# Kernel optimization log

Hardware: AMD Instinct MI355X
Metric: run time of the kernel (lower is better)

The kernel has to match this reference:

```python
import jax, jax.numpy as jnp
import numpy as np

B, D, T = 256, 128, 512
E, H, WH, WIN = 128, 512, 512, 64

def setup_inputs() -> dict:
    key = jax.random.key(0)
    ks = jax.random.split(key, 13)
    def rn(k, shape, scale=0.05):
        return jax.random.normal(k, shape, dtype=jnp.float32) * scale
    return {
        "z_ctx": rn(ks[0], (B, D, WIN), 1.0),
        "z": rn(ks[1], (B, D, T), 1.0),
        "z_slow": rn(ks[2], (B, D, T), 1.0),
        "z_fast": rn(ks[3], (B, D, T), 1.0),
        "e": rn(ks[4], (B, E), 1.0),
        "W_enc": rn(ks[5], (WH, D * WIN)),
        "b_enc": rn(ks[6], (WH,)),
        "W_ih": rn(ks[7], (3 * H, WH + E)),
        "W_hh": rn(ks[8], (3 * H, H)),
        "b_ih": rn(ks[9], (3 * H,)),
        "b_hh": rn(ks[10], (3 * H,)),
        "W_fc": rn(ks[11], (D, H)),
        "b_fc": rn(ks[12], (D,)),
    }

def reference(z_ctx, z, z_slow, z_fast, e, W_enc, b_enc, W_ih, W_hh, b_ih, b_hh, W_fc, b_fc):
    # teacher_forcing=False path (deterministic reference)
    Bb, Dd, Tt = z.shape
    # SlowWindowEncoder: flatten window + Linear + ReLU -> [B, WH]
    context = jax.nn.relu(z_ctx.reshape(Bb, -1) @ W_enc.T + b_enc)
    slow_input = jnp.concatenate([context, e], axis=-1)  # constant over t
    gi = slow_input @ W_ih.T + b_ih                      # [B, 3H], precomputed
    i_r, i_z, i_n = jnp.split(gi, 3, axis=-1)
    Hh = W_hh.shape[1]
    h0 = jnp.zeros((Bb, Hh), dtype=z.dtype)
    zp0 = z_ctx[:, :, -1]                                # z_slow_prev init

    def step(carry, _):
        h, zp = carry
        gh = h @ W_hh.T + b_hh
        h_r, h_z, h_n = jnp.split(gh, 3, axis=-1)
        r = jax.nn.sigmoid(i_r + h_r)
        zg = jax.nn.sigmoid(i_z + h_z)
        n = jnp.tanh(i_n + r * h_n)
        h_new = (1.0 - zg) * n + zg * h                  # GRUCell update
        zh = zp + h_new @ W_fc.T + b_fc                  # residual delta
        return (h_new, zh), zh

    _, zs = jax.lax.scan(step, (h0, zp0), None, length=Tt)  # [T, B, D]
    return jnp.transpose(zs, (1, 2, 0))                  # [B, D, T]
```

## Files before the change

### kernel.cpp

```cpp
#include <hip/hip_runtime.h>

typedef __attribute__((ext_vector_type(8))) short s8v;
typedef __attribute__((ext_vector_type(4))) float f4v;

#define MFMA16(a, b, c) __builtin_amdgcn_mfma_f32_16x16x32_bf16((a), (b), (c), 0, 0, 0)

__device__ __forceinline__ unsigned short f2bf(float f) {
  unsigned u = __float_as_uint(f);
  return (unsigned short)((u + 0x7fffu + ((u >> 16) & 1u)) >> 16);
}

__global__ void cvt4_kernel(const float* __restrict__ in, unsigned short* __restrict__ out, int n4) {
  int i = blockIdx.x * blockDim.x + threadIdx.x;
  if (i >= n4) return;
  float4 v = ((const float4*)in)[i];
  ushort4 o;
  o.x = f2bf(v.x); o.y = f2bf(v.y); o.z = f2bf(v.z); o.w = f2bf(v.w);
  ((ushort4*)out)[i] = o;
}

__global__ void build_slow_kernel(const float* __restrict__ context, const float* __restrict__ e,
                                  unsigned short* __restrict__ out) {
  int i = blockIdx.x * blockDim.x + threadIdx.x;
  if (i >= 256 * 640) return;
  int b = i / 640, c = i - b * 640;
  float v = (c < 512) ? context[b * 512 + c] : e[b * 128 + (c - 512)];
  out[i] = f2bf(v);
}

template <int RELU>
__global__ __launch_bounds__(256) void gemm_bt(const unsigned short* __restrict__ A,
                                               const unsigned short* __restrict__ B,
                                               const float* __restrict__ bias, float* __restrict__ C,
                                               int M, int N, int K) {
  __shared__ unsigned short As[64][48];
  __shared__ unsigned short Bs[64][48];
  int tid = threadIdx.x;
  int lane = tid & 63, w = tid >> 6;
  int m = lane & 15, q = lane >> 4;
  int row0 = blockIdx.x * 64, col0 = blockIdx.y * 64;
  int sr = tid >> 2, sk = (tid & 3) * 8;
  const unsigned short* Ap = A + (size_t)(row0 + sr) * K + sk;
  const unsigned short* Bp = B + (size_t)(col0 + sr) * K + sk;
  f4v acc[4];
#pragma unroll
  for (int nt = 0; nt < 4; nt++) acc[nt] = (f4v){0.f, 0.f, 0.f, 0.f};

  for (int k0 = 0; k0 < K; k0 += 32) {
    *(uint4*)&As[sr][sk] = *(const uint4*)(Ap + k0);
    *(uint4*)&Bs[sr][sk] = *(const uint4*)(Bp + k0);
    __syncthreads();
    s8v a = *(const s8v*)&As[w * 16 + m][q * 8];
#pragma unroll
    for (int nt = 0; nt < 4; nt++) {
      s8v bb = *(const s8v*)&Bs[nt * 16 + m][q * 8];
      acc[nt] = MFMA16(a, bb, acc[nt]);
    }
    __syncthreads();
  }
#pragma unroll
  for (int nt = 0; nt < 4; nt++) {
    int c = col0 + nt * 16 + m;
    float bv = bias[c];
#pragma unroll
    for (int i = 0; i < 4; i++) {
      int r = row0 + w * 16 + q * 4 + i;
      float v = acc[nt][i] + bv;
      if (RELU) v = v > 0.f ? v : 0.f;
      C[(size_t)r * N + c] = v;
    }
  }
}

__global__ __launch_bounds__(64) void gru_scan5(const float* __restrict__ gi,
                                                const unsigned short* __restrict__ Whh,
                                                const float* __restrict__ bhh,
                                                unsigned long long* __restrict__ Hall8,
                                                unsigned int* __restrict__ flags) {
  __shared__ unsigned short wlds[6 * 16 * 64 * 8];
  int tid = threadIdx.x;
  int bid = blockIdx.x;
  int bg = bid >> 4, cg = bid & 15;
  int b0 = bg * 16;
  int n = tid & 15, q = tid >> 4;

#pragma unroll 1
  for (int it = 0; it < 96; ++it) {
    int g = it >> 5, rem = it & 31, ct = rem >> 4, kc = rem & 15;
    int row = g * 512 + cg * 32 + ct * 16 + n;
    int kcol = kc * 32 + q * 8;
    *(uint4*)&wlds[(((g * 2 + ct) * 16 + kc) * 64 + tid) * 8] =
        *(const uint4*)(Whh + (size_t)row * 512 + kcol);
  }

  float gir[2][4], giz[2][4], gin[2][4], bhn[2][4];
#pragma unroll
  for (int ct = 0; ct < 2; ++ct) {
#pragma unroll
    for (int i = 0; i < 4; ++i) {
      int c = cg * 32 + ct * 16 + q * 4 + i;
      const float* gp = gi + (size_t)(b0 + n) * 1536 + c;
      gir[ct][i] = gp[0] + bhh[c];
      giz[ct][i] = gp[512] + bhh[c + 512];
      gin[ct][i] = gp[1024];
      bhn[ct][i] = bhh[c + 1024];
    }
  }
  float hp[2][4] = {{0.f, 0.f, 0.f, 0.f}, {0.f, 0.f, 0.f, 0.f}};
  __syncthreads();

  unsigned int* myflag = flags + bg * 32 + cg;
  const unsigned int* pollp = flags + bg * 32 + (tid & 15);
  size_t rowbase = (size_t)(b0 + n) * 512 * 128;

#pragma unroll 1
  for (int t = 0; t < 512; ++t) {
    f4v ar[2], az[2], an[2];
#pragma unroll
    for (int ct = 0; ct < 2; ++ct) {
      ar[ct] = (f4v){gir[ct][0], gir[ct][1], gir[ct][2], gir[ct][3]};
      az[ct] = (f4v){giz[ct][0], giz[ct][1], giz[ct][2], giz[ct][3]};
      an[ct] = (f4v){bhn[ct][0], bhn[ct][1], bhn[ct][2], bhn[ct][3]};
    }
    if (t > 0) {
      unsigned tgt = (unsigned)t;
      for (long sp = 0; sp < 500000L; ++sp) {
        unsigned v = __hip_atomic_load(pollp, __ATOMIC_RELAXED, __HIP_MEMORY_SCOPE_AGENT);
        if (__ballot(v >= tgt) == 0xffffffffffffffffULL) break;
        if ((sp & 8191) == 8191) __builtin_amdgcn_fence(__ATOMIC_ACQUIRE, "agent");
      }
      asm volatile("" ::: "memory");
      unsigned long long* hp8 = Hall8 + rowbase + (size_t)(t - 1) * 128 + q * 2;
      s8v bf[16];
#pragma unroll
      for (int kc = 0; kc < 16; ++kc) {
        union { unsigned long long u[2]; s8v v; } uv;
        uv.u[0] = __hip_atomic_load(hp8 + kc * 8, __ATOMIC_RELAXED, __HIP_MEMORY_SCOPE_AGENT);
        uv.u[1] = __hip_atomic_load(hp8 + kc * 8 + 1, __ATOMIC_RELAXED, __HIP_MEMORY_SCOPE_AGENT);
        bf[kc] = uv.v;
      }
#pragma unroll
      for (int kc = 0; kc < 16; ++kc) {
#pragma unroll
        for (int ct = 0; ct < 2; ++ct) {
          s8v a0 = *(const s8v*)&wlds[(((0 + ct) * 16 + kc) * 64 + tid) * 8];
          ar[ct] = MFMA16(a0, bf[kc], ar[ct]);
          s8v a1 = *(const s8v*)&wlds[(((2 + ct) * 16 + kc) * 64 + tid) * 8];
          az[ct] = MFMA16(a1, bf[kc], az[ct]);
          s8v a2 = *(const s8v*)&wlds[(((4 + ct) * 16 + kc) * 64 + tid) * 8];
          an[ct] = MFMA16(a2, bf[kc], an[ct]);
        }
      }
    }
#pragma unroll
    for (int ct = 0; ct < 2; ++ct) {
      union { unsigned short s[4]; unsigned long long u; } pk;
#pragma unroll
      for (int i = 0; i < 4; ++i) {
        float r = 1.f / (1.f + __expf(-ar[ct][i]));
        float zg = 1.f / (1.f + __expf(-az[ct][i]));
        float x = gin[ct][i] + r * an[ct][i];
        float ex = __expf(2.f * x);
        float nn = 1.f - 2.f / (ex + 1.f);
        float h = (1.f - zg) * nn + zg * hp[ct][i];
        hp[ct][i] = h;
        pk.s[i] = f2bf(h);
      }
      __hip_atomic_store(Hall8 + rowbase + (size_t)t * 128 + (size_t)(cg * 8 + ct * 4 + q), pk.u,
                         __ATOMIC_RELAXED, __HIP_MEMORY_SCOPE_AGENT);
    }
    asm volatile("s_waitcnt vmcnt(0)" ::: "memory");
    if (tid == 0)
      __hip_atomic_store(myflag, (unsigned int)(t + 1), __ATOMIC_RELAXED,
                         __HIP_MEMORY_SCOPE_AGENT);
  }
}

__global__ __launch_bounds__(256) void fc_scan(const unsigned short* __restrict__ Hall,
                                               const unsigned short* __restrict__ Wfc,
                                               const float* __restrict__ bfc,
                                               const float* __restrict__ zctx,
                                               float* __restrict__ out) {
  __shared__ unsigned short hs[16][520];
  int tid = threadIdx.x;
  int lane = tid & 63, w = tid >> 6;
  int m = lane & 15, q = lane >> 4;
  int b = blockIdx.x;

  s8v wf[2][16];
  float bf_r[2], carry[2];
#pragma unroll
  for (int j = 0; j < 2; j++) {
    int d = (2 * w + j) * 16 + m;
#pragma unroll
    for (int kc = 0; kc < 16; kc++)
      wf[j][kc] = *(const s8v*)(Wfc + (size_t)d * 512 + kc * 32 + q * 8);
    bf_r[j] = bfc[d];
    carry[j] = zctx[((size_t)b * 128 + d) * 64 + 63];
  }

#pragma unroll 1
  for (int chunk = 0; chunk < 32; chunk++) {
    int t0 = chunk * 16;
    {
      int mm = tid >> 4, ci = (tid & 15) * 4;
      const unsigned short* src = Hall + ((size_t)b * 512 + t0 + mm) * 512 + ci * 8;
#pragma unroll
      for (int o = 0; o < 4; o++) {
        uint4 v = *(const uint4*)(src + o * 8);
        *(uint4*)&hs[mm][(ci + o) * 8] = v;
      }
    }
    __syncthreads();
    s8v af[16];
#pragma unroll
    for (int kc = 0; kc < 16; kc++) af[kc] = *(const s8v*)&hs[m][kc * 32 + q * 8];
    f4v acc[2];
    acc[0] = (f4v){0.f, 0.f, 0.f, 0.f};
    acc[1] = (f4v){0.f, 0.f, 0.f, 0.f};
#pragma unroll
    for (int kc = 0; kc < 16; kc++) {
      acc[0] = MFMA16(af[kc], wf[0][kc], acc[0]);
      acc[1] = MFMA16(af[kc], wf[1][kc], acc[1]);
    }
    __syncthreads();

#pragma unroll
    for (int j = 0; j < 2; j++) {
      float s0 = acc[j][0] + bf_r[j];
      float s1 = s0 + acc[j][1] + bf_r[j];
      float s2 = s1 + acc[j][2] + bf_r[j];
      float s3 = s2 + acc[j][3] + bf_r[j];
      float tot = s3;
      float incl = tot;
      float u = __shfl_up(incl, 16, 64);
      if (q >= 1) incl += u;
      u = __shfl_up(incl, 32, 64);
      if (q >= 2) incl += u;
      float excl = incl - tot;
      float add = excl + carry[j];
      int d = (2 * w + j) * 16 + m;
      float4 o4 = make_float4(s0 + add, s1 + add, s2 + add, s3 + add);
      *(float4*)(out + ((size_t)b * 128 + d) * 512 + t0 + q * 4) = o4;
      float chunktot = __shfl(incl, 48 + m, 64);
      carry[j] += chunktot;
    }
  }
}

extern "C" void kernel_launch(void* const* d_in, const int* in_sizes, int n_in,
                              void* d_out, int out_size, void* d_ws, size_t ws_size,
                              hipStream_t stream) {
  const float* z_ctx = (const float*)d_in[0];
  const float* e     = (const float*)d_in[4];
  const float* W_enc = (const float*)d_in[5];
  const float* b_enc = (const float*)d_in[6];
  const float* W_ih  = (const float*)d_in[7];
  const float* W_hh  = (const float*)d_in[8];
  const float* b_ih  = (const float*)d_in[9];
  const float* b_hh  = (const float*)d_in[10];
  const float* W_fc  = (const float*)d_in[11];
  const float* b_fc  = (const float*)d_in[12];
  float* out = (float*)d_out;

  char* ws = (char*)d_ws;
  const size_t OFF_WENC = 0;
  const size_t OFF_ZCTX = 8388608;
  const size_t OFF_WIH  = 12582912;
  const size_t OFF_WHH  = 14548992;
  const size_t OFF_WFC  = 16121856;
  const size_t OFF_CTX  = 16252928;
  const size_t OFF_SLOW = 16777216;
  const size_t OFF_GI   = 17104896;
  const size_t OFF_HALL = 18677760;
  const size_t OFF_SYNC = OFF_HALL + 134217728ull;
  const size_t NEED = OFF_SYNC + 32768;
  if (ws_size < NEED) return;

  unsigned short* Wenc_bf = (unsigned short*)(ws + OFF_WENC);
  unsigned short* zctx_bf = (unsigned short*)(ws + OFF_ZCTX);
  unsigned short* Wih_bf  = (unsigned short*)(ws + OFF_WIH);
  unsigned short* Whh_bf  = (unsigned short*)(ws + OFF_WHH);
  unsigned short* Wfc_bf  = (unsigned short*)(ws + OFF_WFC);
  float* context          = (float*)(ws + OFF_CTX);
  unsigned short* slow_bf = (unsigned short*)(ws + OFF_SLOW);
  float* gi               = (float*)(ws + OFF_GI);
  unsigned short* Hall    = (unsigned short*)(ws + OFF_HALL);
  unsigned long long* Hall8 = (unsigned long long*)(ws + OFF_HALL);
  unsigned int* flags     = (unsigned int*)(ws + OFF_SYNC);

  hipMemsetAsync(flags, 0, 4096, stream);

  cvt4_kernel<<<4096, 256, 0, stream>>>(W_enc, Wenc_bf, 512 * 8192 / 4);
  cvt4_kernel<<<2048, 256, 0, stream>>>(z_ctx, zctx_bf, 256 * 8192 / 4);
  cvt4_kernel<<<960, 256, 0, stream>>>(W_ih, Wih_bf, 1536 * 640 / 4);
  cvt4_kernel<<<768, 256, 0, stream>>>(W_hh, Whh_bf, 1536 * 512 / 4);
  cvt4_kernel<<<64, 256, 0, stream>>>(W_fc, Wfc_bf, 128 * 512 / 4);

  gemm_bt<1><<<dim3(4, 8), 256, 0, stream>>>(zctx_bf, Wenc_bf, b_enc, context, 256, 512, 8192);
  build_slow_kernel<<<640, 256, 0, stream>>>(context, e, slow_bf);
  gemm_bt<0><<<dim3(4, 24), 256, 0, stream>>>(slow_bf, Wih_bf, b_ih, gi, 256, 1536, 640);

  {
    const float* gi_c = gi;
    const unsigned short* whh_c = Whh_bf;
    const float* bhh_c = b_hh;
    unsigned long long* hall_c = Hall8;
    unsigned int* flags_c = flags;
    void* args[] = {(void*)&gi_c, (void*)&whh_c, (void*)&bhh_c, (void*)&hall_c, (void*)&flags_c};
    hipError_t err = hipLaunchCooperativeKernel((void*)gru_scan5, dim3(256), dim3(64), args, 0, stream);
    if (err != hipSuccess) {
      gru_scan5<<<256, 64, 0, stream>>>(gi, Whh_bf, b_hh, Hall8, flags);
    }
  }

  fc_scan<<<256, 256, 0, stream>>>(Hall, Wfc_bf, b_fc, z_ctx, out);
}
```

Before: 2.497 ms.

## Widen GRU scan hidden-state exchange and flag polling to 16-byte cache-bypassing accesses

The recurrent GRU kernel now exchanges hidden state between blocks with 16-byte global loads and stores carrying sc0 sc1 bits, replacing pairs of 8-byte atomics. The permuted K layout of the weights in LDS and in the FC kernel is changed to match, so each lane's packed hidden-state chunk is contiguous. Flag polling now has four lanes each read four flags with one vector load instead of sixteen lanes reading one each, and fences more often. The goal is to cut per-step inter-block synchronisation latency, which dominates the 512 serial steps. In exchange it relies on inline assembly and on memory-ordering assumptions that are not expressed as atomics.

```diff
diff --git a/kernel.cpp b/kernel.cpp
--- a/kernel.cpp
+++ b/kernel.cpp
@@ -2,6 +2,7 @@
 
 typedef __attribute__((ext_vector_type(8))) short s8v;
 typedef __attribute__((ext_vector_type(4))) float f4v;
+typedef __attribute__((ext_vector_type(4))) unsigned int u4v;
 
 #define MFMA16(a, b, c) __builtin_amdgcn_mfma_f32_16x16x32_bf16((a), (b), (c), 0, 0, 0)
 
@@ -72,7 +73,7 @@
   }
 }
 
-__global__ __launch_bounds__(64) void gru_scan5(const float* __restrict__ gi,
+__global__ __launch_bounds__(64) void gru_scan6(const float* __restrict__ gi,
                                                 const unsigned short* __restrict__ Whh,
                                                 const float* __restrict__ bhh,
                                                 unsigned long long* __restrict__ Hall8,
@@ -88,9 +89,10 @@
   for (int it = 0; it < 96; ++it) {
     int g = it >> 5, rem = it & 31, ct = rem >> 4, kc = rem & 15;
     int row = g * 512 + cg * 32 + ct * 16 + n;
-    int kcol = kc * 32 + q * 8;
-    *(uint4*)&wlds[(((g * 2 + ct) * 16 + kc) * 64 + tid) * 8] =
-        *(const uint4*)(Whh + (size_t)row * 512 + kcol);
+    const unsigned short* wb = Whh + (size_t)row * 512 + kc * 32;
+    unsigned short* dst = &wlds[(((g * 2 + ct) * 16 + kc) * 64 + tid) * 8];
+    *(uint2*)dst = *(const uint2*)(wb + q * 4);
+    *(uint2*)(dst + 4) = *(const uint2*)(wb + 16 + q * 4);
   }
 
   float gir[2][4], giz[2][4], gin[2][4], bhn[2][4];
@@ -110,7 +112,7 @@
   __syncthreads();
 
   unsigned int* myflag = flags + bg * 32 + cg;
-  const unsigned int* pollp = flags + bg * 32 + (tid & 15);
+  const unsigned int* pollp = flags + bg * 32 + (tid & 3) * 4;
   size_t rowbase = (size_t)(b0 + n) * 512 * 128;
 
 #pragma unroll 1
@@ -125,20 +127,31 @@
     if (t > 0) {
       unsigned tgt = (unsigned)t;
       for (long sp = 0; sp < 500000L; ++sp) {
-        unsigned v = __hip_atomic_load(pollp, __ATOMIC_RELAXED, __HIP_MEMORY_SCOPE_AGENT);
-        if (__ballot(v >= tgt) == 0xffffffffffffffffULL) break;
-        if ((sp & 8191) == 8191) __builtin_amdgcn_fence(__ATOMIC_ACQUIRE, "agent");
+        unsigned m0 = tgt, m1 = tgt, m2 = tgt, m3 = tgt;
+        if (tid < 4) {
+          u4v fv;
+          asm volatile("global_load_dwordx4 %0, %1, off sc0 sc1\n\ts_waitcnt vmcnt(0)"
+                       : "=v"(fv)
+                       : "v"(pollp)
+                       : "memory");
+          m0 = fv[0]; m1 = fv[1]; m2 = fv[2]; m3 = fv[3];
+        }
+        bool ok = (m0 >= tgt) && (m1 >= tgt) && (m2 >= tgt) && (m3 >= tgt);
+        if (__ballot(ok) == 0xffffffffffffffffULL) break;
+        if ((sp & 63) == 63) __builtin_amdgcn_fence(__ATOMIC_ACQUIRE, "agent");
       }
       asm volatile("" ::: "memory");
-      unsigned long long* hp8 = Hall8 + rowbase + (size_t)(t - 1) * 128 + q * 2;
+      const char* hb = (const char*)(Hall8 + rowbase + (size_t)(t - 1) * 128) + q * 16;
       s8v bf[16];
 #pragma unroll
       for (int kc = 0; kc < 16; ++kc) {
-        union { unsigned long long u[2]; s8v v; } uv;
-        uv.u[0] = __hip_atomic_load(hp8 + kc * 8, __ATOMIC_RELAXED, __HIP_MEMORY_SCOPE_AGENT);
-        uv.u[1] = __hip_atomic_load(hp8 + kc * 8 + 1, __ATOMIC_RELAXED, __HIP_MEMORY_SCOPE_AGENT);
-        bf[kc] = uv.v;
-      }
+        asm volatile("global_load_dwordx4 %0, %1, off sc0 sc1"
+                     : "=v"(bf[kc])
+                     : "v"(hb + (size_t)kc * 64)
+                     : "memory");
+      }
+      asm volatile("s_waitcnt vmcnt(0)" ::: "memory");
+      __builtin_amdgcn_sched_barrier(0);
 #pragma unroll
       for (int kc = 0; kc < 16; ++kc) {
 #pragma unroll
@@ -152,6 +165,7 @@
         }
       }
     }
+    unsigned long long hu[2];
 #pragma unroll
     for (int ct = 0; ct < 2; ++ct) {
       union { unsigned short s[4]; unsigned long long u; } pk;
@@ -166,13 +180,22 @@
         hp[ct][i] = h;
         pk.s[i] = f2bf(h);
       }
-      __hip_atomic_store(Hall8 + rowbase + (size_t)t * 128 + (size_t)(cg * 8 + ct * 4 + q), pk.u,
-                         __ATOMIC_RELAXED, __HIP_MEMORY_SCOPE_AGENT);
+      hu[ct] = pk.u;
+    }
+    {
+      u4v stv;
+      stv[0] = (unsigned)hu[0];
+      stv[1] = (unsigned)(hu[0] >> 32);
+      stv[2] = (unsigned)hu[1];
+      stv[3] = (unsigned)(hu[1] >> 32);
+      unsigned long long* hstp = Hall8 + rowbase + (size_t)t * 128 + (size_t)(cg * 8 + q * 2);
+      asm volatile("global_store_dwordx4 %0, %1, off sc0 sc1" ::"v"(hstp), "v"(stv) : "memory");
     }
     asm volatile("s_waitcnt vmcnt(0)" ::: "memory");
-    if (tid == 0)
-      __hip_atomic_store(myflag, (unsigned int)(t + 1), __ATOMIC_RELAXED,
-                         __HIP_MEMORY_SCOPE_AGENT);
+    if (tid == 0) {
+      unsigned fv = (unsigned)(t + 1);
+      asm volatile("global_store_dword %0, %1, off sc0 sc1" ::"v"(myflag), "v"(fv) : "memory");
+    }
   }
 }
 
@@ -193,8 +216,13 @@
   for (int j = 0; j < 2; j++) {
     int d = (2 * w + j) * 16 + m;
 #pragma unroll
-    for (int kc = 0; kc < 16; kc++)
-      wf[j][kc] = *(const s8v*)(Wfc + (size_t)d * 512 + kc * 32 + q * 8);
+    for (int kc = 0; kc < 16; kc++) {
+      const unsigned short* wb = Wfc + (size_t)d * 512 + kc * 32;
+      union { uint2 u2[2]; s8v v; } wu;
+      wu.u2[0] = *(const uint2*)(wb + q * 4);
+      wu.u2[1] = *(const uint2*)(wb + 16 + q * 4);
+      wf[j][kc] = wu.v;
+    }
     bf_r[j] = bfc[d];
     carry[j] = zctx[((size_t)b * 128 + d) * 64 + 63];
   }
@@ -308,9 +336,9 @@
     unsigned long long* hall_c = Hall8;
     unsigned int* flags_c = flags;
     void* args[] = {(void*)&gi_c, (void*)&whh_c, (void*)&bhh_c, (void*)&hall_c, (void*)&flags_c};
-    hipError_t err = hipLaunchCooperativeKernel((void*)gru_scan5, dim3(256), dim3(64), args, 0, stream);
+    hipError_t err = hipLaunchCooperativeKernel((void*)gru_scan6, dim3(256), dim3(64), args, 0, stream);
     if (err != hipSuccess) {
-      gru_scan5<<<256, 64, 0, stream>>>(gi, Whh_bf, b_hh, Hall8, flags);
+      gru_scan6<<<256, 64, 0, stream>>>(gi, Whh_bf, b_hh, Hall8, flags);
     }
   }
 
```

Result: slower. 2.660 ms (+6.6%).

## Use sentinel-filled hidden-state buffer to drop store wait before flag publish

Applied to the files above, without the earlier changes.

The full hidden-state history buffer is pre-filled with 0xFF so consumers can detect rows that have not arrived yet. The s_waitcnt vmcnt(0) before the per-step flag store is removed, and readers instead re-poll any 32-bit word still holding the sentinel pattern. This is meant to shorten the per-step producer critical path in the recurrent scan, at the cost of a 128 MB memset each call and a retry loop on the consumer side. It could misfire if a real packed bf16 pair ever equals 0xFFFFFFFF (a NaN pattern).

```diff
diff --git a/kernel.cpp b/kernel.cpp
--- a/kernel.cpp
+++ b/kernel.cpp
@@ -72,11 +72,11 @@
   }
 }
 
-__global__ __launch_bounds__(64) void gru_scan5(const float* __restrict__ gi,
-                                                const unsigned short* __restrict__ Whh,
-                                                const float* __restrict__ bhh,
-                                                unsigned long long* __restrict__ Hall8,
-                                                unsigned int* __restrict__ flags) {
+__global__ __launch_bounds__(64) void gru_scan10(const float* __restrict__ gi,
+                                                 const unsigned short* __restrict__ Whh,
+                                                 const float* __restrict__ bhh,
+                                                 unsigned long long* __restrict__ Hall8,
+                                                 unsigned int* __restrict__ flags) {
   __shared__ unsigned short wlds[6 * 16 * 64 * 8];
   int tid = threadIdx.x;
   int bid = blockIdx.x;
@@ -131,24 +131,41 @@
       }
       asm volatile("" ::: "memory");
       unsigned long long* hp8 = Hall8 + rowbase + (size_t)(t - 1) * 128 + q * 2;
-      s8v bf[16];
+      unsigned long long u0[16], u1[16];
+#pragma unroll
+      for (int kc = 0; kc < 16; ++kc) {
+        u0[kc] = __hip_atomic_load(hp8 + kc * 8, __ATOMIC_RELAXED, __HIP_MEMORY_SCOPE_AGENT);
+        u1[kc] = __hip_atomic_load(hp8 + kc * 8 + 1, __ATOMIC_RELAXED, __HIP_MEMORY_SCOPE_AGENT);
+      }
+      for (long rp = 0; rp < 100000L; ++rp) {
+        bool bad = false;
+#pragma unroll
+        for (int kc = 0; kc < 16; ++kc) {
+          if ((unsigned)u0[kc] == 0xFFFFFFFFu || (unsigned)(u0[kc] >> 32) == 0xFFFFFFFFu) {
+            u0[kc] = __hip_atomic_load(hp8 + kc * 8, __ATOMIC_RELAXED, __HIP_MEMORY_SCOPE_AGENT);
+            bad = true;
+          }
+          if ((unsigned)u1[kc] == 0xFFFFFFFFu || (unsigned)(u1[kc] >> 32) == 0xFFFFFFFFu) {
+            u1[kc] = __hip_atomic_load(hp8 + kc * 8 + 1, __ATOMIC_RELAXED, __HIP_MEMORY_SCOPE_AGENT);
+            bad = true;
+          }
+        }
+        if (__ballot(bad) == 0ULL) break;
+      }
 #pragma unroll
       for (int kc = 0; kc < 16; ++kc) {
         union { unsigned long long u[2]; s8v v; } uv;
-        uv.u[0] = __hip_atomic_load(hp8 + kc * 8, __ATOMIC_RELAXED, __HIP_MEMORY_SCOPE_AGENT);
-        uv.u[1] = __hip_atomic_load(hp8 + kc * 8 + 1, __ATOMIC_RELAXED, __HIP_MEMORY_SCOPE_AGENT);
-        bf[kc] = uv.v;
-      }
-#pragma unroll
-      for (int kc = 0; kc < 16; ++kc) {
+        uv.u[0] = u0[kc];
+        uv.u[1] = u1[kc];
+        s8v bfv = uv.v;
 #pragma unroll
         for (int ct = 0; ct < 2; ++ct) {
           s8v a0 = *(const s8v*)&wlds[(((0 + ct) * 16 + kc) * 64 + tid) * 8];
-          ar[ct] = MFMA16(a0, bf[kc], ar[ct]);
+          ar[ct] = MFMA16(a0, bfv, ar[ct]);
           s8v a1 = *(const s8v*)&wlds[(((2 + ct) * 16 + kc) * 64 + tid) * 8];
-          az[ct] = MFMA16(a1, bf[kc], az[ct]);
+          az[ct] = MFMA16(a1, bfv, az[ct]);
           s8v a2 = *(const s8v*)&wlds[(((4 + ct) * 16 + kc) * 64 + tid) * 8];
-          an[ct] = MFMA16(a2, bf[kc], an[ct]);
+          an[ct] = MFMA16(a2, bfv, an[ct]);
         }
       }
     }
@@ -169,7 +186,6 @@
       __hip_atomic_store(Hall8 + rowbase + (size_t)t * 128 + (size_t)(cg * 8 + ct * 4 + q), pk.u,
                          __ATOMIC_RELAXED, __HIP_MEMORY_SCOPE_AGENT);
     }
-    asm volatile("s_waitcnt vmcnt(0)" ::: "memory");
     if (tid == 0)
       __hip_atomic_store(myflag, (unsigned int)(t + 1), __ATOMIC_RELAXED,
                          __HIP_MEMORY_SCOPE_AGENT);
@@ -273,7 +289,8 @@
   const size_t OFF_SLOW = 16777216;
   const size_t OFF_GI   = 17104896;
   const size_t OFF_HALL = 18677760;
-  const size_t OFF_SYNC = OFF_HALL + 134217728ull;
+  const size_t HALL_SZ  = 134217728ull;
+  const size_t OFF_SYNC = OFF_HALL + HALL_SZ;
   const size_t NEED = OFF_SYNC + 32768;
   if (ws_size < NEED) return;
 
@@ -289,7 +306,8 @@
   unsigned long long* Hall8 = (unsigned long long*)(ws + OFF_HALL);
   unsigned int* flags     = (unsigned int*)(ws + OFF_SYNC);
 
-  hipMemsetAsync(flags, 0, 4096, stream);
+  (void)hipMemsetAsync(Hall, 0xFF, HALL_SZ, stream);
+  (void)hipMemsetAsync(flags, 0, 4096, stream);
 
   cvt4_kernel<<<4096, 256, 0, stream>>>(W_enc, Wenc_bf, 512 * 8192 / 4);
   cvt4_kernel<<<2048, 256, 0, stream>>>(z_ctx, zctx_bf, 256 * 8192 / 4);
@@ -308,9 +326,9 @@
     unsigned long long* hall_c = Hall8;
     unsigned int* flags_c = flags;
     void* args[] = {(void*)&gi_c, (void*)&whh_c, (void*)&bhh_c, (void*)&hall_c, (void*)&flags_c};
-    hipError_t err = hipLaunchCooperativeKernel((void*)gru_scan5, dim3(256), dim3(64), args, 0, stream);
+    hipError_t err = hipLaunchCooperativeKernel((void*)gru_scan10, dim3(256), dim3(64), args, 0, stream);
     if (err != hipSuccess) {
-      gru_scan5<<<256, 64, 0, stream>>>(gi, Whh_bf, b_hh, Hall8, flags);
+      gru_scan10<<<256, 64, 0, stream>>>(gi, Whh_bf, b_hh, Hall8, flags);
     }
   }
 
```

Result: slower. 2.823 ms (+13.1%).
